# Optimization experiments

Measured on AMD Instinct MI355X. Metric: run time of the kernel, lower is better.

## Reference

```python
import jax, jax.numpy as jnp
import numpy as np

B, H, W = 8, 128, 128
DIM, HEADS, WS, FF = 192, 8, 8, 2
EPS = 1e-6
HD = DIM // HEADS
L = WS * WS
SCALE = HD ** -0.5


def _rel_index(ws):
    coord = np.stack(np.meshgrid(np.arange(ws), np.arange(ws), indexing='ij')).reshape(2, -1)
    rel = (coord[:, :, None] - coord[:, None, :]).transpose(1, 2, 0)
    rel[..., 0] += ws - 1
    rel[..., 1] += ws - 1
    rel[..., 0] *= 2 * ws - 1
    return rel.sum(-1)

REL_INDEX = jnp.asarray(_rel_index(WS))  # (L, L) int


def _part(x):
    # (B,C,H,W) -> (B*nH*nW, L, C)
    b, c, h, w = x.shape
    x = x.reshape(b, c, h // WS, WS, w // WS, WS).transpose(0, 2, 4, 3, 5, 1)
    return x.reshape(-1, L, c)


def _merge(xw, c):
    # (B*nH*nW, L, C) -> (B,C,H,W)
    x = xw.reshape(B, H // WS, W // WS, WS, WS, c).transpose(0, 5, 1, 3, 2, 4)
    return x.reshape(B, c, H, W)


def _forward(x_rgb, x_sar, gamma, beta, ln1_w, ln1_b, ln2_w, ln2_b,
             qkv_w, qkv_b, attn_proj_w, attn_proj_b, rel_bias,
             q_w, kv_w, cross_proj_w, cross_proj_b, ffn_w1, ffn_w2):
    def cln(x, w, b_):
        # conditional LayerNorm over channel dim
        mu = x.mean(axis=1, keepdims=True)
        var = ((x - mu) ** 2).mean(axis=1, keepdims=True)
        xn = (x - mu) * jax.lax.rsqrt(var + EPS)
        xn = xn * w[None, :, None, None] + b_[None, :, None, None]
        return gamma[:, :, None, None] * xn + beta[:, :, None, None]

    def mh(t):  # (n,L,C) -> (n,L,H,hd)
        return t.reshape(t.shape[0], L, HEADS, HD)

    # --- window self-attention with relative position bias ---
    xw = _part(cln(x_rgb, ln1_w, ln1_b))
    qkv = xw @ qkv_w.T + qkv_b
    q, k, v = jnp.split(qkv, 3, axis=-1)
    att = jnp.einsum('nqhd,nkhd->nhqk', mh(q), mh(k)) * SCALE
    bias = rel_bias[REL_INDEX].transpose(2, 0, 1)[None]  # (1,H,L,L)
    att = jax.nn.softmax(att + bias, axis=-1)
    o = jnp.einsum('nhqk,nkhd->nqhd', att, mh(v)).reshape(-1, L, DIM)
    y = jnp.einsum('bchw,oc->bohw', _merge(o, DIM), attn_proj_w) + attn_proj_b[None, :, None, None]
    x1 = x_rgb + y

    # --- windowed cross-attention (q from rgb branch, kv from sar) ---
    qw = _part(cln(x1, ln1_w, ln1_b)) @ q_w.T
    kc, vc = jnp.split(_part(x_sar) @ kv_w.T, 2, axis=-1)
    att2 = jax.nn.softmax(jnp.einsum('nqhd,nkhd->nhqk', mh(qw), mh(kc)) * SCALE, axis=-1)
    o2 = jnp.einsum('nhqk,nkhd->nqhd', att2, mh(vc)).reshape(-1, L, DIM)
    y2 = jnp.einsum('bchw,oc->bohw', _merge(o2, DIM), cross_proj_w) + cross_proj_b[None, :, None, None]
    x2 = x1 + y2

    # --- conv(1x1)-GELU-conv(1x1) FFN ---
    hdn = jax.nn.gelu(jnp.einsum('bchw,oc->bohw', cln(x2, ln2_w, ln2_b), ffn_w1), approximate=False)
    y3 = jnp.einsum('bchw,oc->bohw', hdn, ffn_w2)
    return x2 + y3


def setup_inputs() -> dict:
    key = jax.random.key(0)
    ks = jax.random.split(key, 12)
    d = DIM

    def n(k, shape, s=0.02):
        return jax.random.normal(k, shape, dtype=jnp.float32) * s

    return {
        'x_rgb': jax.random.normal(ks[0], (B, d, H, W), dtype=jnp.float32),
        'x_sar': jax.random.normal(ks[1], (B, d, H, W), dtype=jnp.float32),
        'gamma': jax.random.normal(ks[2], (B, d), dtype=jnp.float32),
        'beta': jax.random.normal(ks[3], (B, d), dtype=jnp.float32),
        'ln1_w': jnp.ones((d,), jnp.float32), 'ln1_b': jnp.zeros((d,), jnp.float32),
        'ln2_w': jnp.ones((d,), jnp.float32), 'ln2_b': jnp.zeros((d,), jnp.float32),
        'qkv_w': n(ks[4], (3 * d, d)), 'qkv_b': jnp.zeros((3 * d,), jnp.float32),
        'attn_proj_w': n(ks[5], (d, d)), 'attn_proj_b': jnp.zeros((d,), jnp.float32),
        'rel_bias': n(ks[6], ((2 * WS - 1) ** 2, HEADS)),
        'q_w': n(ks[7], (d, d)), 'kv_w': n(ks[8], (2 * d, d)),
        'cross_proj_w': n(ks[9], (d, d)), 'cross_proj_b': jnp.zeros((d,), jnp.float32),
        'ffn_w1': n(ks[10], (d * FF * 2, d)), 'ffn_w2': n(ks[11], (d, d * FF * 2)),
    }


def reference(x_rgb, x_sar, gamma, beta, ln1_w, ln1_b, ln2_w, ln2_b,
              qkv_w, qkv_b, attn_proj_w, attn_proj_b, rel_bias,
              q_w, kv_w, cross_proj_w, cross_proj_b, ffn_w1, ffn_w2):
    return _forward(x_rgb, x_sar, gamma, beta, ln1_w, ln1_b, ln2_w, ln2_b,
                    qkv_w, qkv_b, attn_proj_w, attn_proj_b, rel_bias,
                    q_w, kv_w, cross_proj_w, cross_proj_b, ffn_w1, ffn_w2)
```

## Files before the change

### kernel.cpp

```cpp
#include <hip/hip_runtime.h>
#include <math.h>


#define TPB 256
#define TPB2 512
#define NWIN 2048
#define SCALEF 0.20412414523193154f

typedef __attribute__((ext_vector_type(8))) short bhalf8;
typedef __attribute__((ext_vector_type(4))) float fvec4;

#define MFMA(a, b, c) __builtin_amdgcn_mfma_f32_16x16x32_bf16(a, b, c, 0, 0, 0)

__device__ __forceinline__ short f2bf(float f) {
    unsigned u = __float_as_uint(f);
    u = u + 0x7fffu + ((u >> 16) & 1u);
    return (short)(u >> 16);
}
__device__ __forceinline__ float bf2f(short s) {
    return __uint_as_float(((unsigned)(unsigned short)s) << 16);
}

#define N_QKV 147456
#define N_QC  49152
#define N_KV  98304
#define N_AP  36864
#define N_CP  36864
#define N_W1  147456
#define N_W2  147456
#define W_TOT 663552

#define PW 7424

__global__ __launch_bounds__(TPB) void k0_wprep(
    const float* __restrict__ qkvw, const float* __restrict__ qkvb,
    const float* __restrict__ qw, const float* __restrict__ kvw,
    const float* __restrict__ apw, const float* __restrict__ cpw,
    const float* __restrict__ w1, const float* __restrict__ w2,
    short* __restrict__ Wqkv, short* __restrict__ Wqc, short* __restrict__ Wkv,
    short* __restrict__ Wap, short* __restrict__ Wcp, short* __restrict__ W1b,
    short* __restrict__ W2b, float* __restrict__ qbp)
{
    const int tid = blockIdx.x * TPB + threadIdx.x;
    const int stride = gridDim.x * TPB;
    for (int i = tid; i < N_QKV; i += stride) {
        int tile = i >> 9, pos = i & 511;
        int lane = pos >> 3, j = pos & 7, l16 = lane & 15, g = lane >> 4;
        int h = tile / 36, t2 = tile % 36, nt = t2 / 6, kt = t2 % 6;
        int col = nt * 16 + l16, sub = col >> 5, d = col & 31;
        int k = kt * 32 + g * 8 + j;
        float v = (d < 24) ? qkvw[(sub * 192 + h * 24 + d) * 192 + k] : 0.f;
        Wqkv[i] = f2bf(v);
    }
    for (int i = tid; i < N_QC; i += stride) {
        int tile = i >> 9, pos = i & 511;
        int lane = pos >> 3, j = pos & 7, l16 = lane & 15, g = lane >> 4;
        int h = tile / 12, t2 = tile % 12, nt = t2 / 6, kt = t2 % 6;
        int col = nt * 16 + l16;
        int k = kt * 32 + g * 8 + j;
        float v = (col < 24) ? qw[(h * 24 + col) * 192 + k] : 0.f;
        Wqc[i] = f2bf(v);
    }
    for (int i = tid; i < N_KV; i += stride) {
        int tile = i >> 9, pos = i & 511;
        int lane = pos >> 3, j = pos & 7, l16 = lane & 15, g = lane >> 4;
        int h = tile / 24, t2 = tile % 24, nt = t2 / 6, kt = t2 % 6;
        int col = nt * 16 + l16, sub = col >> 5, d = col & 31;
        int k = kt * 32 + g * 8 + j;
        float v = (d < 24) ? kvw[(sub * 192 + h * 24 + d) * 192 + k] : 0.f;
        Wkv[i] = f2bf(v);
    }
    for (int i = tid; i < N_AP; i += stride) {
        int tile = i >> 9, pos = i & 511;
        int lane = pos >> 3, j = pos & 7, l16 = lane & 15, g = lane >> 4;
        int nt = tile / 6, kt = tile % 6;
        int n = nt * 16 + l16, k = kt * 32 + g * 8 + j;
        Wap[i] = f2bf(apw[n * 192 + k]);
    }
    for (int i = tid; i < N_CP; i += stride) {
        int tile = i >> 9, pos = i & 511;
        int lane = pos >> 3, j = pos & 7, l16 = lane & 15, g = lane >> 4;
        int nt = tile / 6, kt = tile % 6;
        int n = nt * 16 + l16, k = kt * 32 + g * 8 + j;
        Wcp[i] = f2bf(cpw[n * 192 + k]);
    }
    for (int i = tid; i < N_W1; i += stride) {
        int tile = i >> 9, pos = i & 511;
        int lane = pos >> 3, j = pos & 7, l16 = lane & 15, g = lane >> 4;
        int nt = tile / 6, kt = tile % 6;
        int n = nt * 16 + l16, k = kt * 32 + g * 8 + j;
        W1b[i] = f2bf(w1[n * 192 + k]);
    }
    for (int i = tid; i < N_W2; i += stride) {
        int tile = i >> 9, pos = i & 511;
        int lane = pos >> 3, j = pos & 7, l16 = lane & 15, g = lane >> 4;
        int nt = tile / 24, ks = tile % 24;
        int n = nt * 16 + l16, k = ks * 32 + g * 8 + j;
        W2b[i] = f2bf(w2[n * 768 + k]);
    }
    for (int i = tid; i < 768; i += stride) {
        int h = i / 96, col = i % 96, sub = col >> 5, d = col & 31;
        qbp[i] = (d < 24) ? qkvb[sub * 192 + h * 24 + d] : 0.f;
    }
}

__global__ __launch_bounds__(TPB) void k1_prep(
    const float* __restrict__ xrgb, const float* __restrict__ xsar,
    const float* __restrict__ gamma, const float* __restrict__ beta,
    const float* __restrict__ ln1w, const float* __restrict__ ln1b,
    short* __restrict__ Ag, short* __restrict__ Xg, short* __restrict__ Sg)
{
    __shared__ float s_x[64 * 193];
    __shared__ float s_mu[64], s_rs[64];
    __shared__ float s_cw[768];
    const int tid = threadIdx.x;
    const int wid = blockIdx.x;
    const int b = wid >> 8, hb = (wid >> 4) & 15, wb = wid & 15;
    const int xbase = ((b * 192) << 14) + ((hb * 8) << 7) + wb * 8;
    const int tok0 = wid * 12288;

    for (int i = tid; i < 192; i += TPB) {
        s_cw[i]       = ln1w[i];
        s_cw[192 + i] = ln1b[i];
        s_cw[384 + i] = gamma[b * 192 + i];
        s_cw[576 + i] = beta[b * 192 + i];
    }
    for (int i = tid; i < 3072; i += TPB) {
        int c = i >> 4, rem = i & 15, hrow = rem >> 1, half = rem & 1;
        float4 v = *(const float4*)&xrgb[xbase + (c << 14) + (hrow << 7) + half * 4];
        int l = hrow * 8 + half * 4;
        s_x[(l + 0) * 193 + c] = v.x;
        s_x[(l + 1) * 193 + c] = v.y;
        s_x[(l + 2) * 193 + c] = v.z;
        s_x[(l + 3) * 193 + c] = v.w;
    }
    __syncthreads();
    {
        int t = tid >> 2, q4 = tid & 3;
        float sum = 0.f, sq = 0.f;
        for (int j = 0; j < 48; j++) {
            float v = s_x[t * 193 + q4 * 48 + j];
            sum += v; sq += v * v;
        }
        sum += __shfl_xor(sum, 1); sum += __shfl_xor(sum, 2);
        sq  += __shfl_xor(sq, 1);  sq  += __shfl_xor(sq, 2);
        float mu = sum * (1.f / 192.f);
        float var = sq * (1.f / 192.f) - mu * mu;
        if (q4 == 0) { s_mu[t] = mu; s_rs[t] = rsqrtf(var + 1e-6f); }
    }
    __syncthreads();
    for (int i = tid; i < 1536; i += TPB) {
        int flat = i << 3, t = flat / 192, c0 = flat - t * 192;
        float mu = s_mu[t], rs = s_rs[t];
        bhalf8 xv, av;
#pragma unroll
        for (int j = 0; j < 8; j++) {
            float x = s_x[t * 193 + c0 + j];
            xv[j] = f2bf(x);
            float xn = (x - mu) * rs;
            av[j] = f2bf((xn * s_cw[c0 + j] + s_cw[192 + c0 + j]) * s_cw[384 + c0 + j] + s_cw[576 + c0 + j]);
        }
        *(bhalf8*)&Xg[tok0 + flat] = xv;
        *(bhalf8*)&Ag[tok0 + flat] = av;
    }
    __syncthreads();
    for (int i = tid; i < 3072; i += TPB) {
        int c = i >> 4, rem = i & 15, hrow = rem >> 1, half = rem & 1;
        float4 v = *(const float4*)&xsar[xbase + (c << 14) + (hrow << 7) + half * 4];
        int l = hrow * 8 + half * 4;
        s_x[(l + 0) * 193 + c] = v.x;
        s_x[(l + 1) * 193 + c] = v.y;
        s_x[(l + 2) * 193 + c] = v.z;
        s_x[(l + 3) * 193 + c] = v.w;
    }
    __syncthreads();
    for (int i = tid; i < 1536; i += TPB) {
        int flat = i << 3, t = flat / 192, c0 = flat - t * 192;
        bhalf8 sv;
#pragma unroll
        for (int j = 0; j < 8; j++) sv[j] = f2bf(s_x[t * 193 + c0 + j]);
        *(bhalf8*)&Sg[tok0 + flat] = sv;
    }
}

__global__ __launch_bounds__(TPB2, 2) void k2_self(
    short* __restrict__ Ag, short* __restrict__ Xg,
    const short* __restrict__ Wqkv, const float* __restrict__ qbp,
    const short* __restrict__ Wap, const float* __restrict__ apb,
    const float* __restrict__ relb,
    const float* __restrict__ ln1w, const float* __restrict__ ln1b,
    const float* __restrict__ gamma, const float* __restrict__ beta)
{
    __shared__ short s_a[12800];
    __shared__ short s_w8[8 * PW];
    __shared__ short s_rb[1800];
    __shared__ float s_part[512];
    __shared__ float s_mv[128];

    const int tid = threadIdx.x;
    const int wid = blockIdx.x;
    const int b = wid >> 8;
    const int w = tid >> 6;
    const int lane = tid & 63;
    const int g = lane >> 4;
    const int l16 = lane & 15;
    const int fo = lane << 3;
    const int tok0 = wid * 12288;
    short* const sq  = &s_w8[w * PW];
    short* const sk  = sq + 2560;
    short* const svt = sq + 5120;
    short* const sp  = sq;
    short* const so  = sq;
    const fvec4 z4 = {0.f, 0.f, 0.f, 0.f};

#pragma unroll
    for (int t = 0; t < 3; t++) {
        int i = tid + t * TPB2;
        int flat = i << 3, row = flat / 192, col = flat - row * 192;
        *(bhalf8*)&s_a[row * 200 + col] = *(const bhalf8*)&Ag[tok0 + flat];
    }
    for (int i = tid; i < 1800; i += TPB2) s_rb[i] = f2bf(relb[i]);
    __syncthreads();

    {
        const int h = w;
        fvec4 acc[4][6];
#pragma unroll
        for (int mt = 0; mt < 4; mt++)
#pragma unroll
            for (int nt = 0; nt < 6; nt++) acc[mt][nt] = z4;
        __builtin_amdgcn_s_setprio(1);
#pragma unroll
        for (int kt = 0; kt < 6; kt++) {
            bhalf8 af[4];
#pragma unroll
            for (int mt = 0; mt < 4; mt++)
                af[mt] = *(const bhalf8*)&s_a[(mt * 16 + l16) * 200 + kt * 32 + g * 8];
#pragma unroll
            for (int nt = 0; nt < 6; nt++) {
                bhalf8 wf = *(const bhalf8*)&Wqkv[((h * 36 + nt * 6 + kt) << 9) + fo];
#pragma unroll
                for (int mt = 0; mt < 4; mt++)
                    acc[mt][nt] = MFMA(af[mt], wf, acc[mt][nt]);
            }
        }
        __builtin_amdgcn_s_setprio(0);
#pragma unroll
        for (int nt = 0; nt < 6; nt++) {
            float bq = qbp[h * 96 + nt * 16 + l16];
            int d = (nt & 1) * 16 + l16;
#pragma unroll
            for (int mt = 0; mt < 4; mt++)
#pragma unroll
                for (int r = 0; r < 4; r++) {
                    int tok = mt * 16 + g * 4 + r;
                    short bv = f2bf(acc[mt][nt][r] + bq);
                    if (nt < 2)      sq[tok * 40 + d] = bv;
                    else if (nt < 4) sk[tok * 40 + d] = bv;
                    else             svt[d * 72 + tok] = bv;
                }
        }
        fvec4 sacc[4][4];
        {
            bhalf8 qf[4], kf[4];
#pragma unroll
            for (int mt = 0; mt < 4; mt++)
                qf[mt] = *(const bhalf8*)&sq[(mt * 16 + l16) * 40 + g * 8];
#pragma unroll
            for (int nt = 0; nt < 4; nt++)
                kf[nt] = *(const bhalf8*)&sk[(nt * 16 + l16) * 40 + g * 8];
#pragma unroll
            for (int mt = 0; mt < 4; mt++)
#pragma unroll
                for (int nt = 0; nt < 4; nt++)
                    sacc[mt][nt] = MFMA(qf[mt], kf[nt], z4);
        }
#pragma unroll
        for (int mt = 0; mt < 4; mt++) {
            float sv[4][4];
#pragma unroll
            for (int nt = 0; nt < 4; nt++) {
                int n = nt * 16 + l16, ki = n >> 3, kj = n & 7;
#pragma unroll
                for (int r = 0; r < 4; r++) {
                    int qq = mt * 16 + g * 4 + r, qi = qq >> 3, qj = qq & 7;
                    int ridx = (qi - ki + 7) * 15 + (qj - kj + 7);
                    sv[nt][r] = sacc[mt][nt][r] * SCALEF + bf2f(s_rb[ridx * 8 + h]);
                }
            }
#pragma unroll
            for (int r = 0; r < 4; r++) {
                float m = fmaxf(fmaxf(sv[0][r], sv[1][r]), fmaxf(sv[2][r], sv[3][r]));
                m = fmaxf(m, __shfl_xor(m, 1)); m = fmaxf(m, __shfl_xor(m, 2));
                m = fmaxf(m, __shfl_xor(m, 4)); m = fmaxf(m, __shfl_xor(m, 8));
                float s = 0.f;
#pragma unroll
                for (int nt = 0; nt < 4; nt++) { sv[nt][r] = __expf(sv[nt][r] - m); s += sv[nt][r]; }
                s += __shfl_xor(s, 1); s += __shfl_xor(s, 2);
                s += __shfl_xor(s, 4); s += __shfl_xor(s, 8);
                float inv = 1.f / s;
#pragma unroll
                for (int nt = 0; nt < 4; nt++)
                    sp[(mt * 16 + g * 4 + r) * 72 + nt * 16 + l16] = f2bf(sv[nt][r] * inv);
            }
        }
        fvec4 oacc[4][2];
#pragma unroll
        for (int mt = 0; mt < 4; mt++) { oacc[mt][0] = z4; oacc[mt][1] = z4; }
#pragma unroll
        for (int ks = 0; ks < 2; ks++) {
            bhalf8 pf[4];
#pragma unroll
            for (int mt = 0; mt < 4; mt++)
                pf[mt] = *(const bhalf8*)&sp[(mt * 16 + l16) * 72 + ks * 32 + g * 8];
#pragma unroll
            for (int nt = 0; nt < 2; nt++) {
                bhalf8 vf = *(const bhalf8*)&svt[(nt * 16 + l16) * 72 + ks * 32 + g * 8];
#pragma unroll
                for (int mt = 0; mt < 4; mt++)
                    oacc[mt][nt] = MFMA(pf[mt], vf, oacc[mt][nt]);
            }
        }
#pragma unroll
        for (int nt = 0; nt < 2; nt++) {
            int d = nt * 16 + l16;
            if (d < 24) {
#pragma unroll
                for (int mt = 0; mt < 4; mt++)
#pragma unroll
                    for (int r = 0; r < 4; r++)
                        so[(mt * 16 + g * 4 + r) * 24 + d] = f2bf(oacc[mt][nt][r]);
            }
        }
    }
    __syncthreads();

    bhalf8 xst[3]; int xr[3], xc[3];
#pragma unroll
    for (int t = 0; t < 3; t++) {
        int i = tid + t * TPB2;
        int flat = i << 3; xr[t] = flat / 192; xc[t] = flat - xr[t] * 192;
        xst[t] = *(const bhalf8*)&Xg[tok0 + flat];
    }

    const int mh = w & 1, ng = w >> 1;
    fvec4 p[2][3];
#pragma unroll
    for (int m = 0; m < 2; m++)
#pragma unroll
        for (int j = 0; j < 3; j++) p[m][j] = z4;
#pragma unroll
    for (int kt = 0; kt < 6; kt++) {
        int c0 = kt * 32 + g * 8;
        int h0 = c0 / 24, d0 = c0 - h0 * 24;
        bhalf8 of[2];
#pragma unroll
        for (int m = 0; m < 2; m++)
            of[m] = *(const bhalf8*)&s_w8[h0 * PW + ((mh * 2 + m) * 16 + l16) * 24 + d0];
#pragma unroll
        for (int j = 0; j < 3; j++) {
            bhalf8 wf = *(const bhalf8*)&Wap[(((ng * 3 + j) * 6 + kt) << 9) + fo];
#pragma unroll
            for (int m = 0; m < 2; m++)
                p[m][j] = MFMA(of[m], wf, p[m][j]);
        }
    }
#pragma unroll
    for (int t = 0; t < 3; t++)
        *(bhalf8*)&s_a[xr[t] * 200 + xc[t]] = xst[t];
    __syncthreads();

    float xv[2][3][4];
#pragma unroll
    for (int j = 0; j < 3; j++) {
        int col = ng * 48 + j * 16 + l16;
        float ap = apb[col];
#pragma unroll
        for (int m = 0; m < 2; m++)
#pragma unroll
            for (int r = 0; r < 4; r++) {
                int row = (mh * 2 + m) * 16 + g * 4 + r;
                xv[m][j][r] = bf2f(s_a[row * 200 + col]) + p[m][j][r] + ap;
            }
    }
#pragma unroll
    for (int m = 0; m < 2; m++)
#pragma unroll
        for (int r = 0; r < 4; r++) {
            float s1 = xv[m][0][r] + xv[m][1][r] + xv[m][2][r];
            float s2 = xv[m][0][r] * xv[m][0][r] + xv[m][1][r] * xv[m][1][r] + xv[m][2][r] * xv[m][2][r];
            s1 += __shfl_xor(s1, 1); s1 += __shfl_xor(s1, 2); s1 += __shfl_xor(s1, 4); s1 += __shfl_xor(s1, 8);
            s2 += __shfl_xor(s2, 1); s2 += __shfl_xor(s2, 2); s2 += __shfl_xor(s2, 4); s2 += __shfl_xor(s2, 8);
            if (l16 == 0) {
                int row = (mh * 2 + m) * 16 + g * 4 + r;
                s_part[(ng * 64 + row) * 2]     = s1;
                s_part[(ng * 64 + row) * 2 + 1] = s2;
            }
        }
    __syncthreads();
    if (tid < 64) {
        float s1 = s_part[tid * 2] + s_part[(64 + tid) * 2] + s_part[(128 + tid) * 2] + s_part[(192 + tid) * 2];
        float s2 = s_part[tid * 2 + 1] + s_part[(64 + tid) * 2 + 1] + s_part[(128 + tid) * 2 + 1] + s_part[(192 + tid) * 2 + 1];
        float mu = s1 * (1.f / 192.f);
        float var = s2 * (1.f / 192.f) - mu * mu;
        s_mv[tid * 2] = mu;
        s_mv[tid * 2 + 1] = rsqrtf(var + 1e-6f);
    }
    __syncthreads();
#pragma unroll
    for (int j = 0; j < 3; j++) {
        int col = ng * 48 + j * 16 + l16;
        float lw = ln1w[col], lb = ln1b[col], ga = gamma[b * 192 + col], be = beta[b * 192 + col];
#pragma unroll
        for (int m = 0; m < 2; m++)
#pragma unroll
            for (int r = 0; r < 4; r++) {
                int row = (mh * 2 + m) * 16 + g * 4 + r;
                float x = xv[m][j][r];
                s_a[row * 200 + col] = f2bf(x);
                float xn = (x - s_mv[row * 2]) * s_mv[row * 2 + 1];
                s_w8[row * 200 + col] = f2bf((xn * lw + lb) * ga + be);
            }
    }
    __syncthreads();
#pragma unroll
    for (int t = 0; t < 3; t++) {
        int i = tid + t * TPB2;
        int flat = i << 3, row = flat / 192, col = flat - row * 192;
        *(bhalf8*)&Xg[tok0 + flat] = *(const bhalf8*)&s_a[row * 200 + col];
        *(bhalf8*)&Ag[tok0 + flat] = *(const bhalf8*)&s_w8[row * 200 + col];
    }
}

__global__ __launch_bounds__(TPB2, 2) void k3_cross(
    short* __restrict__ Ag, short* __restrict__ Xg, const short* __restrict__ Sg,
    const short* __restrict__ Wqc, const short* __restrict__ Wkv,
    const short* __restrict__ Wcp, const float* __restrict__ cpb,
    const float* __restrict__ ln2w, const float* __restrict__ ln2b,
    const float* __restrict__ gamma, const float* __restrict__ beta)
{
    __shared__ short s_s[12800];
    __shared__ short s_w8[8 * PW];
    __shared__ float s_part[512];
    __shared__ float s_mv[128];

    const int tid = threadIdx.x;
    const int wid = blockIdx.x;
    const int b = wid >> 8;
    const int w = tid >> 6;
    const int lane = tid & 63;
    const int g = lane >> 4;
    const int l16 = lane & 15;
    const int fo = lane << 3;
    const int tok0 = wid * 12288;
    short* const sq  = &s_w8[w * PW];
    short* const sk  = sq + 2560;
    short* const svt = sq + 5120;
    short* const sp  = sq;
    short* const so  = sq;
    const fvec4 z4 = {0.f, 0.f, 0.f, 0.f};

#pragma unroll
    for (int t = 0; t < 3; t++) {
        int i = tid + t * TPB2;
        int flat = i << 3, row = flat / 192, col = flat - row * 192;
        *(bhalf8*)&s_s[row * 200 + col] = *(const bhalf8*)&Sg[tok0 + flat];
    }
    __syncthreads();

    {
        const int h = w;
        fvec4 acc[4][6];
#pragma unroll
        for (int mt = 0; mt < 4; mt++)
#pragma unroll
            for (int nt = 0; nt < 6; nt++) acc[mt][nt] = z4;
        __builtin_amdgcn_s_setprio(1);
#pragma unroll
        for (int kt = 0; kt < 6; kt++) {
            bhalf8 ag[4], sf[4];
#pragma unroll
            for (int mt = 0; mt < 4; mt++) {
                ag[mt] = *(const bhalf8*)&Ag[tok0 + (mt * 16 + l16) * 192 + kt * 32 + g * 8];
                sf[mt] = *(const bhalf8*)&s_s[(mt * 16 + l16) * 200 + kt * 32 + g * 8];
            }
#pragma unroll
            for (int nt = 0; nt < 2; nt++) {
                bhalf8 wf = *(const bhalf8*)&Wqc[((h * 12 + nt * 6 + kt) << 9) + fo];
#pragma unroll
                for (int mt = 0; mt < 4; mt++)
                    acc[mt][nt] = MFMA(ag[mt], wf, acc[mt][nt]);
            }
#pragma unroll
            for (int nt = 0; nt < 2; nt++) {
                bhalf8 wf = *(const bhalf8*)&Wkv[((h * 24 + nt * 6 + kt) << 9) + fo];
#pragma unroll
                for (int mt = 0; mt < 4; mt++)
                    acc[mt][2 + nt] = MFMA(sf[mt], wf, acc[mt][2 + nt]);
            }
#pragma unroll
            for (int nt = 0; nt < 2; nt++) {
                bhalf8 wf = *(const bhalf8*)&Wkv[((h * 24 + (nt + 2) * 6 + kt) << 9) + fo];
#pragma unroll
                for (int mt = 0; mt < 4; mt++)
                    acc[mt][4 + nt] = MFMA(sf[mt], wf, acc[mt][4 + nt]);
            }
        }
        __builtin_amdgcn_s_setprio(0);
#pragma unroll
        for (int nt = 0; nt < 6; nt++) {
            int d = (nt & 1) * 16 + l16;
#pragma unroll
            for (int mt = 0; mt < 4; mt++)
#pragma unroll
                for (int r = 0; r < 4; r++) {
                    int tok = mt * 16 + g * 4 + r;
                    short bv = f2bf(acc[mt][nt][r]);
                    if (nt < 2)      sq[tok * 40 + d] = bv;
                    else if (nt < 4) sk[tok * 40 + d] = bv;
                    else             svt[d * 72 + tok] = bv;
                }
        }
        fvec4 sacc[4][4];
        {
            bhalf8 qf[4], kf[4];
#pragma unroll
            for (int mt = 0; mt < 4; mt++)
                qf[mt] = *(const bhalf8*)&sq[(mt * 16 + l16) * 40 + g * 8];
#pragma unroll
            for (int nt = 0; nt < 4; nt++)
                kf[nt] = *(const bhalf8*)&sk[(nt * 16 + l16) * 40 + g * 8];
#pragma unroll
            for (int mt = 0; mt < 4; mt++)
#pragma unroll
                for (int nt = 0; nt < 4; nt++)
                    sacc[mt][nt] = MFMA(qf[mt], kf[nt], z4);
        }
#pragma unroll
        for (int mt = 0; mt < 4; mt++) {
            float sv[4][4];
#pragma unroll
            for (int nt = 0; nt < 4; nt++)
#pragma unroll
                for (int r = 0; r < 4; r++)
                    sv[nt][r] = sacc[mt][nt][r] * SCALEF;
#pragma unroll
            for (int r = 0; r < 4; r++) {
                float m = fmaxf(fmaxf(sv[0][r], sv[1][r]), fmaxf(sv[2][r], sv[3][r]));
                m = fmaxf(m, __shfl_xor(m, 1)); m = fmaxf(m, __shfl_xor(m, 2));
                m = fmaxf(m, __shfl_xor(m, 4)); m = fmaxf(m, __shfl_xor(m, 8));
                float s = 0.f;
#pragma unroll
                for (int nt = 0; nt < 4; nt++) { sv[nt][r] = __expf(sv[nt][r] - m); s += sv[nt][r]; }
                s += __shfl_xor(s, 1); s += __shfl_xor(s, 2);
                s += __shfl_xor(s, 4); s += __shfl_xor(s, 8);
                float inv = 1.f / s;
#pragma unroll
                for (int nt = 0; nt < 4; nt++)
                    sp[(mt * 16 + g * 4 + r) * 72 + nt * 16 + l16] = f2bf(sv[nt][r] * inv);
            }
        }
        fvec4 oacc[4][2];
#pragma unroll
        for (int mt = 0; mt < 4; mt++) { oacc[mt][0] = z4; oacc[mt][1] = z4; }
#pragma unroll
        for (int ks = 0; ks < 2; ks++) {
            bhalf8 pf[4];
#pragma unroll
            for (int mt = 0; mt < 4; mt++)
                pf[mt] = *(const bhalf8*)&sp[(mt * 16 + l16) * 72 + ks * 32 + g * 8];
#pragma unroll
            for (int nt = 0; nt < 2; nt++) {
                bhalf8 vf = *(const bhalf8*)&svt[(nt * 16 + l16) * 72 + ks * 32 + g * 8];
#pragma unroll
                for (int mt = 0; mt < 4; mt++)
                    oacc[mt][nt] = MFMA(pf[mt], vf, oacc[mt][nt]);
            }
        }
#pragma unroll
        for (int nt = 0; nt < 2; nt++) {
            int d = nt * 16 + l16;
            if (d < 24) {
#pragma unroll
                for (int mt = 0; mt < 4; mt++)
#pragma unroll
                    for (int r = 0; r < 4; r++)
                        so[(mt * 16 + g * 4 + r) * 24 + d] = f2bf(oacc[mt][nt][r]);
            }
        }
    }
    __syncthreads();

    bhalf8 xst[3]; int xr[3], xc[3];
#pragma unroll
    for (int t = 0; t < 3; t++) {
        int i = tid + t * TPB2;
        int flat = i << 3; xr[t] = flat / 192; xc[t] = flat - xr[t] * 192;
        xst[t] = *(const bhalf8*)&Xg[tok0 + flat];
    }

    const int mh = w & 1, ng = w >> 1;
    fvec4 p[2][3];
#pragma unroll
    for (int m = 0; m < 2; m++)
#pragma unroll
        for (int j = 0; j < 3; j++) p[m][j] = z4;
#pragma unroll
    for (int kt = 0; kt < 6; kt++) {
        int c0 = kt * 32 + g * 8;
        int h0 = c0 / 24, d0 = c0 - h0 * 24;
        bhalf8 of[2];
#pragma unroll
        for (int m = 0; m < 2; m++)
            of[m] = *(const bhalf8*)&s_w8[h0 * PW + ((mh * 2 + m) * 16 + l16) * 24 + d0];
#pragma unroll
        for (int j = 0; j < 3; j++) {
            bhalf8 wf = *(const bhalf8*)&Wcp[(((ng * 3 + j) * 6 + kt) << 9) + fo];
#pragma unroll
            for (int m = 0; m < 2; m++)
                p[m][j] = MFMA(of[m], wf, p[m][j]);
        }
    }
#pragma unroll
    for (int t = 0; t < 3; t++)
        *(bhalf8*)&s_s[xr[t] * 200 + xc[t]] = xst[t];
    __syncthreads();

    float xv[2][3][4];
#pragma unroll
    for (int j = 0; j < 3; j++) {
        int col = ng * 48 + j * 16 + l16;
        float cp = cpb[col];
#pragma unroll
        for (int m = 0; m < 2; m++)
#pragma unroll
            for (int r = 0; r < 4; r++) {
                int row = (mh * 2 + m) * 16 + g * 4 + r;
                xv[m][j][r] = bf2f(s_s[row * 200 + col]) + p[m][j][r] + cp;
            }
    }
#pragma unroll
    for (int m = 0; m < 2; m++)
#pragma unroll
        for (int r = 0; r < 4; r++) {
            float s1 = xv[m][0][r] + xv[m][1][r] + xv[m][2][r];
            float s2 = xv[m][0][r] * xv[m][0][r] + xv[m][1][r] * xv[m][1][r] + xv[m][2][r] * xv[m][2][r];
            s1 += __shfl_xor(s1, 1); s1 += __shfl_xor(s1, 2); s1 += __shfl_xor(s1, 4); s1 += __shfl_xor(s1, 8);
            s2 += __shfl_xor(s2, 1); s2 += __shfl_xor(s2, 2); s2 += __shfl_xor(s2, 4); s2 += __shfl_xor(s2, 8);
            if (l16 == 0) {
                int row = (mh * 2 + m) * 16 + g * 4 + r;
                s_part[(ng * 64 + row) * 2]     = s1;
                s_part[(ng * 64 + row) * 2 + 1] = s2;
            }
        }
    __syncthreads();
    if (tid < 64) {
        float s1 = s_part[tid * 2] + s_part[(64 + tid) * 2] + s_part[(128 + tid) * 2] + s_part[(192 + tid) * 2];
        float s2 = s_part[tid * 2 + 1] + s_part[(64 + tid) * 2 + 1] + s_part[(128 + tid) * 2 + 1] + s_part[(192 + tid) * 2 + 1];
        float mu = s1 * (1.f / 192.f);
        float var = s2 * (1.f / 192.f) - mu * mu;
        s_mv[tid * 2] = mu;
        s_mv[tid * 2 + 1] = rsqrtf(var + 1e-6f);
    }
    __syncthreads();
#pragma unroll
    for (int j = 0; j < 3; j++) {
        int col = ng * 48 + j * 16 + l16;
        float lw = ln2w[col], lb = ln2b[col], ga = gamma[b * 192 + col], be = beta[b * 192 + col];
#pragma unroll
        for (int m = 0; m < 2; m++)
#pragma unroll
            for (int r = 0; r < 4; r++) {
                int row = (mh * 2 + m) * 16 + g * 4 + r;
                float x = xv[m][j][r];
                s_s[row * 200 + col] = f2bf(x);
                float xn = (x - s_mv[row * 2]) * s_mv[row * 2 + 1];
                s_w8[row * 200 + col] = f2bf((xn * lw + lb) * ga + be);
            }
    }
    __syncthreads();
#pragma unroll
    for (int t = 0; t < 3; t++) {
        int i = tid + t * TPB2;
        int flat = i << 3, row = flat / 192, col = flat - row * 192;
        *(bhalf8*)&Xg[tok0 + flat] = *(const bhalf8*)&s_s[row * 200 + col];
        *(bhalf8*)&Ag[tok0 + flat] = *(const bhalf8*)&s_w8[row * 200 + col];
    }
}

__global__ __launch_bounds__(TPB) void k4_ffn(
    const short* __restrict__ Ag, const short* __restrict__ Xg,
    const short* __restrict__ W1b, const short* __restrict__ W2b,
    float* __restrict__ out)
{
    __shared__ short s_u[12800];
    __shared__ short s_h[12800];

    const int tid = threadIdx.x;
    const int wid = blockIdx.x;
    const int b = wid >> 8, hb = (wid >> 4) & 15, wb = wid & 15;
    const int xbase = ((b * 192) << 14) + ((hb * 8) << 7) + wb * 8;
    const int w = tid >> 6;
    const int lane = tid & 63;
    const int g = lane >> 4;
    const int l16 = lane & 15;
    const int fo = lane << 3;
    const int tok0 = wid * 12288;
    const fvec4 z4 = {0.f, 0.f, 0.f, 0.f};

    for (int i = tid; i < 1536; i += TPB) {
        int flat = i << 3;
        int t = flat / 192, cc = flat - t * 192;
        *(bhalf8*)&s_u[t * 200 + cc] = *(const bhalf8*)&Ag[tok0 + flat];
    }
    bhalf8 xpre[6];
#pragma unroll
    for (int t6 = 0; t6 < 6; t6++)
        xpre[t6] = *(const bhalf8*)&Xg[tok0 + ((tid + t6 * TPB) << 3)];
    __syncthreads();

    fvec4 yacc[4][3];
#pragma unroll
    for (int mt = 0; mt < 4; mt++)
#pragma unroll
        for (int j = 0; j < 3; j++) yacc[mt][j] = z4;

    for (int c = 0; c < 6; c++) {
        fvec4 hacc[4][2];
#pragma unroll
        for (int mt = 0; mt < 4; mt++) { hacc[mt][0] = z4; hacc[mt][1] = z4; }
#pragma unroll
        for (int kt = 0; kt < 6; kt++) {
            bhalf8 af[4];
#pragma unroll
            for (int mt = 0; mt < 4; mt++)
                af[mt] = *(const bhalf8*)&s_u[(mt * 16 + l16) * 200 + kt * 32 + g * 8];
#pragma unroll
            for (int n2 = 0; n2 < 2; n2++) {
                bhalf8 wf = *(const bhalf8*)&W1b[(((c * 8 + w * 2 + n2) * 6 + kt) << 9) + fo];
#pragma unroll
                for (int mt = 0; mt < 4; mt++)
                    hacc[mt][n2] = MFMA(af[mt], wf, hacc[mt][n2]);
            }
        }
#pragma unroll
        for (int n2 = 0; n2 < 2; n2++) {
            int cc = w * 32 + n2 * 16 + l16;
#pragma unroll
            for (int mt = 0; mt < 4; mt++) {
#pragma unroll
                for (int r = 0; r < 4; r++) {
                    float x = hacc[mt][n2][r];
                    float z = 1.5957691216f * x * (1.f + 0.044715f * x * x);
                    float gl = x / (1.f + __expf(-z));
                    s_h[(mt * 16 + g * 4 + r) * 200 + cc] = f2bf(gl);
                }
            }
        }
        __syncthreads();
#pragma unroll
        for (int ks = 0; ks < 4; ks++) {
            bhalf8 hf[4];
#pragma unroll
            for (int mt = 0; mt < 4; mt++)
                hf[mt] = *(const bhalf8*)&s_h[(mt * 16 + l16) * 200 + ks * 32 + g * 8];
#pragma unroll
            for (int j = 0; j < 3; j++) {
                bhalf8 wf = *(const bhalf8*)&W2b[(((w * 3 + j) * 24 + c * 4 + ks) << 9) + fo];
#pragma unroll
                for (int mt = 0; mt < 4; mt++)
                    yacc[mt][j] = MFMA(hf[mt], wf, yacc[mt][j]);
            }
        }
        __syncthreads();
    }

#pragma unroll
    for (int t6 = 0; t6 < 6; t6++) {
        int i = tid + t6 * TPB;
        int flat = i << 3;
        int t = flat / 192, cc = flat - t * 192;
        *(bhalf8*)&s_h[t * 200 + cc] = xpre[t6];
    }
    __syncthreads();
#pragma unroll
    for (int j = 0; j < 3; j++) {
        int col = (w * 3 + j) * 16 + l16;
#pragma unroll
        for (int mt = 0; mt < 4; mt++) {
#pragma unroll
            for (int r = 0; r < 4; r++) {
                int tok = mt * 16 + g * 4 + r;
                float v = bf2f(s_h[tok * 200 + col]) + yacc[mt][j][r];
                s_u[tok * 200 + col] = f2bf(v);
            }
        }
    }
    __syncthreads();
    for (int i = tid; i < 3072; i += TPB) {
        int cc = i >> 4, rem = i & 15, hrow = rem >> 1, half = rem & 1;
        int l0 = hrow * 8 + half * 4;
        float4 v;
        v.x = bf2f(s_u[(l0 + 0) * 200 + cc]);
        v.y = bf2f(s_u[(l0 + 1) * 200 + cc]);
        v.z = bf2f(s_u[(l0 + 2) * 200 + cc]);
        v.w = bf2f(s_u[(l0 + 3) * 200 + cc]);
        *(float4*)&out[xbase + (cc << 14) + (hrow << 7) + half * 4] = v;
    }
}

extern "C" void kernel_launch(void* const* d_in, const int* in_sizes, int n_in,
                              void* d_out, int out_size, void* d_ws, size_t ws_size,
                              hipStream_t stream) {
    const float* xrgb  = (const float*)d_in[0];
    const float* xsar  = (const float*)d_in[1];
    const float* gamma = (const float*)d_in[2];
    const float* beta  = (const float*)d_in[3];
    const float* ln1w  = (const float*)d_in[4];
    const float* ln1b  = (const float*)d_in[5];
    const float* ln2w  = (const float*)d_in[6];
    const float* ln2b  = (const float*)d_in[7];
    const float* qkvw  = (const float*)d_in[8];
    const float* qkvb  = (const float*)d_in[9];
    const float* apw   = (const float*)d_in[10];
    const float* apb   = (const float*)d_in[11];
    const float* relb  = (const float*)d_in[12];
    const float* qw    = (const float*)d_in[13];
    const float* kvw   = (const float*)d_in[14];
    const float* cpw   = (const float*)d_in[15];
    const float* cpb   = (const float*)d_in[16];
    const float* w1    = (const float*)d_in[17];
    const float* w2    = (const float*)d_in[18];

    char* base = (char*)d_ws;
    short* Wqkv = (short*)base;
    short* Wqc  = Wqkv + N_QKV;
    short* Wkv  = Wqc + N_QC;
    short* Wap  = Wkv + N_KV;
    short* Wcp  = Wap + N_AP;
    short* W1b  = Wcp + N_CP;
    short* W2b  = W1b + N_W1;
    float* qbp  = (float*)(base + (size_t)W_TOT * 2);
    short* Ag   = (short*)(base + (size_t)W_TOT * 2 + 3072);
    short* Xg   = Ag + 25165824;
    short* Sg   = Xg + 25165824;

    float* out = (float*)d_out;

    hipLaunchKernelGGL(k0_wprep, dim3(256), dim3(TPB), 0, stream,
                       qkvw, qkvb, qw, kvw, apw, cpw, w1, w2,
                       Wqkv, Wqc, Wkv, Wap, Wcp, W1b, W2b, qbp);
    hipLaunchKernelGGL(k1_prep, dim3(NWIN), dim3(TPB), 0, stream,
                       xrgb, xsar, gamma, beta, ln1w, ln1b, Ag, Xg, Sg);
    hipLaunchKernelGGL(k2_self, dim3(NWIN), dim3(TPB2), 0, stream,
                       Ag, Xg, Wqkv, qbp, Wap, apb, relb, ln1w, ln1b, gamma, beta);
    hipLaunchKernelGGL(k3_cross, dim3(NWIN), dim3(TPB2), 0, stream,
                       Ag, Xg, Sg, Wqc, Wkv, Wcp, cpb, ln2w, ln2b, gamma, beta);
    hipLaunchKernelGGL(k4_ffn, dim3(NWIN), dim3(TPB), 0, stream,
                       Ag, Xg, W1b, W2b, out);
}
```

Measured before the change: 978.6 us.

## Run FFN kernel with 512 threads and split work across eight waves

The FFN kernel now launches 512 threads (8 waves) per window instead of 256. Each wave computes one 16-column slice of the hidden chunk in the first GEMM, and the second GEMM is split into two row halves by three column groups. The hidden buffer shrinks to a 136-element pitch, and the residual is now read from global memory after the loop instead of being prefetched into registers. This is meant to raise parallelism and occupancy and cut register pressure. The cost is more waves per barrier and a scalar, non-vectorized final output store.

Result: faster. 897.6 us (-8.3%).

```diff
diff --git a/kernel.cpp b/kernel.cpp
--- a/kernel.cpp
+++ b/kernel.cpp
@@ -688,13 +688,13 @@
     }
 }
 
-__global__ __launch_bounds__(TPB) void k4_ffn(
+__global__ __launch_bounds__(TPB2, 6) void k4_ffn(
     const short* __restrict__ Ag, const short* __restrict__ Xg,
     const short* __restrict__ W1b, const short* __restrict__ W2b,
     float* __restrict__ out)
 {
     __shared__ short s_u[12800];
-    __shared__ short s_h[12800];
+    __shared__ short s_h[8704];
 
     const int tid = threadIdx.x;
     const int wid = blockIdx.x;
@@ -706,106 +706,91 @@
     const int l16 = lane & 15;
     const int fo = lane << 3;
     const int tok0 = wid * 12288;
+    const int mh = w & 1, ng = w >> 1;
     const fvec4 z4 = {0.f, 0.f, 0.f, 0.f};
 
-    for (int i = tid; i < 1536; i += TPB) {
-        int flat = i << 3;
-        int t = flat / 192, cc = flat - t * 192;
-        *(bhalf8*)&s_u[t * 200 + cc] = *(const bhalf8*)&Ag[tok0 + flat];
-    }
-    bhalf8 xpre[6];
-#pragma unroll
-    for (int t6 = 0; t6 < 6; t6++)
-        xpre[t6] = *(const bhalf8*)&Xg[tok0 + ((tid + t6 * TPB) << 3)];
-    __syncthreads();
-
-    fvec4 yacc[4][3];
-#pragma unroll
-    for (int mt = 0; mt < 4; mt++)
-#pragma unroll
-        for (int j = 0; j < 3; j++) yacc[mt][j] = z4;
+#pragma unroll
+    for (int t = 0; t < 3; t++) {
+        int i = tid + t * TPB2;
+        int flat = i << 3, row = flat / 192, col = flat - row * 192;
+        *(bhalf8*)&s_u[row * 200 + col] = *(const bhalf8*)&Ag[tok0 + flat];
+    }
+    __syncthreads();
+
+    fvec4 yacc[2][3];
+#pragma unroll
+    for (int m = 0; m < 2; m++)
+#pragma unroll
+        for (int j = 0; j < 3; j++) yacc[m][j] = z4;
 
     for (int c = 0; c < 6; c++) {
-        fvec4 hacc[4][2];
-#pragma unroll
-        for (int mt = 0; mt < 4; mt++) { hacc[mt][0] = z4; hacc[mt][1] = z4; }
+        fvec4 hacc[4];
+#pragma unroll
+        for (int mt = 0; mt < 4; mt++) hacc[mt] = z4;
 #pragma unroll
         for (int kt = 0; kt < 6; kt++) {
-            bhalf8 af[4];
-#pragma unroll
-            for (int mt = 0; mt < 4; mt++)
-                af[mt] = *(const bhalf8*)&s_u[(mt * 16 + l16) * 200 + kt * 32 + g * 8];
-#pragma unroll
-            for (int n2 = 0; n2 < 2; n2++) {
-                bhalf8 wf = *(const bhalf8*)&W1b[(((c * 8 + w * 2 + n2) * 6 + kt) << 9) + fo];
-#pragma unroll
-                for (int mt = 0; mt < 4; mt++)
-                    hacc[mt][n2] = MFMA(af[mt], wf, hacc[mt][n2]);
-            }
-        }
-#pragma unroll
-        for (int n2 = 0; n2 < 2; n2++) {
-            int cc = w * 32 + n2 * 16 + l16;
+            bhalf8 wf = *(const bhalf8*)&W1b[(((c * 8 + w) * 6 + kt) << 9) + fo];
 #pragma unroll
             for (int mt = 0; mt < 4; mt++) {
+                bhalf8 af = *(const bhalf8*)&s_u[(mt * 16 + l16) * 200 + kt * 32 + g * 8];
+                hacc[mt] = MFMA(af, wf, hacc[mt]);
+            }
+        }
+        {
+            int cc = w * 16 + l16;
+#pragma unroll
+            for (int mt = 0; mt < 4; mt++) {
 #pragma unroll
                 for (int r = 0; r < 4; r++) {
-                    float x = hacc[mt][n2][r];
+                    float x = hacc[mt][r];
                     float z = 1.5957691216f * x * (1.f + 0.044715f * x * x);
                     float gl = x / (1.f + __expf(-z));
-                    s_h[(mt * 16 + g * 4 + r) * 200 + cc] = f2bf(gl);
+                    s_h[(mt * 16 + g * 4 + r) * 136 + cc] = f2bf(gl);
                 }
             }
         }
         __syncthreads();
 #pragma unroll
         for (int ks = 0; ks < 4; ks++) {
-            bhalf8 hf[4];
-#pragma unroll
-            for (int mt = 0; mt < 4; mt++)
-                hf[mt] = *(const bhalf8*)&s_h[(mt * 16 + l16) * 200 + ks * 32 + g * 8];
+            bhalf8 hf[2];
+#pragma unroll
+            for (int m = 0; m < 2; m++)
+                hf[m] = *(const bhalf8*)&s_h[((mh * 2 + m) * 16 + l16) * 136 + ks * 32 + g * 8];
 #pragma unroll
             for (int j = 0; j < 3; j++) {
-                bhalf8 wf = *(const bhalf8*)&W2b[(((w * 3 + j) * 24 + c * 4 + ks) << 9) + fo];
-#pragma unroll
-                for (int mt = 0; mt < 4; mt++)
-                    yacc[mt][j] = MFMA(hf[mt], wf, yacc[mt][j]);
+                bhalf8 wf = *(const bhalf8*)&W2b[(((ng * 3 + j) * 24 + c * 4 + ks) << 9) + fo];
+#pragma unroll
+                for (int m = 0; m < 2; m++)
+                    yacc[m][j] = MFMA(hf[m], wf, yacc[m][j]);
             }
         }
         __syncthreads();
     }
 
 #pragma unroll
-    for (int t6 = 0; t6 < 6; t6++) {
-        int i = tid + t6 * TPB;
-        int flat = i << 3;
-        int t = flat / 192, cc = flat - t * 192;
-        *(bhalf8*)&s_h[t * 200 + cc] = xpre[t6];
+    for (int t = 0; t < 3; t++) {
+        int i = tid + t * TPB2;
+        int flat = i << 3, row = flat / 192, col = flat - row * 192;
+        *(bhalf8*)&s_u[row * 200 + col] = *(const bhalf8*)&Xg[tok0 + flat];
     }
     __syncthreads();
 #pragma unroll
     for (int j = 0; j < 3; j++) {
-        int col = (w * 3 + j) * 16 + l16;
-#pragma unroll
-        for (int mt = 0; mt < 4; mt++) {
+        int col = ng * 48 + j * 16 + l16;
+#pragma unroll
+        for (int m = 0; m < 2; m++) {
 #pragma unroll
             for (int r = 0; r < 4; r++) {
-                int tok = mt * 16 + g * 4 + r;
-                float v = bf2f(s_h[tok * 200 + col]) + yacc[mt][j][r];
+                int tok = (mh * 2 + m) * 16 + g * 4 + r;
+                float v = bf2f(s_u[tok * 200 + col]) + yacc[m][j][r];
                 s_u[tok * 200 + col] = f2bf(v);
             }
         }
     }
     __syncthreads();
-    for (int i = tid; i < 3072; i += TPB) {
-        int cc = i >> 4, rem = i & 15, hrow = rem >> 1, half = rem & 1;
-        int l0 = hrow * 8 + half * 4;
-        float4 v;
-        v.x = bf2f(s_u[(l0 + 0) * 200 + cc]);
-        v.y = bf2f(s_u[(l0 + 1) * 200 + cc]);
-        v.z = bf2f(s_u[(l0 + 2) * 200 + cc]);
-        v.w = bf2f(s_u[(l0 + 3) * 200 + cc]);
-        *(float4*)&out[xbase + (cc << 14) + (hrow << 7) + half * 4] = v;
+    for (int i = tid; i < 12288; i += TPB2) {
+        int cc = i >> 6, l = i & 63;
+        out[xbase + (cc << 14) + ((l >> 3) << 7) + (l & 7)] = bf2f(s_u[l * 200 + cc]);
     }
 }
 
@@ -856,6 +841,6 @@
                        Ag, Xg, Wqkv, qbp, Wap, apb, relb, ln1w, ln1b, gamma, beta);
     hipLaunchKernelGGL(k3_cross, dim3(NWIN), dim3(TPB2), 0, stream,
                        Ag, Xg, Sg, Wqc, Wkv, Wcp, cpb, ln2w, ln2b, gamma, beta);
-    hipLaunchKernelGGL(k4_ffn, dim3(NWIN), dim3(TPB), 0, stream,
+    hipLaunchKernelGGL(k4_ffn, dim3(NWIN), dim3(TPB2), 0, stream,
                        Ag, Xg, W1b, W2b, out);
 }
```
